# Optimization experiments

Measured on AMD Instinct MI355X. Metric: run time of the kernel, lower is better.

Reference implementation:

```python
import jax, jax.numpy as jnp
import numpy as np

BS, SEQ, VOCAB, EMS, NHID, ML = 32, 512, 5000, 256, 512, 16
TEMP = 0.9
GAMMA = 0.0  # self.gamma is a fixed zero Variable in the original


def setup_inputs() -> dict:
    key = jax.random.key(0)
    ks = jax.random.split(key, 10)
    nm = SEQ // ML
    inputs = jax.random.randint(ks[0], (BS, SEQ), 0, VOCAB, dtype=jnp.int32)
    measure_steps = jax.random.randint(ks[1], (ML, BS, nm), 0, VOCAB, dtype=jnp.int32)
    measure_weights = jax.random.normal(ks[2], (BS, nm, nm), dtype=jnp.float32)
    h0 = jnp.zeros((BS, NHID), jnp.float32)
    c0 = jnp.zeros((BS, NHID), jnp.float32)
    initrange = 0.1
    emb = jax.random.uniform(ks[3], (VOCAB, EMS), minval=-initrange, maxval=initrange)
    k = 1.0 / np.sqrt(NHID).astype(np.float32)
    W_ih = jax.random.uniform(ks[4], (4 * NHID, EMS), minval=-k, maxval=k)
    W_hh = jax.random.uniform(ks[5], (4 * NHID, NHID), minval=-k, maxval=k)
    b_ih = jax.random.uniform(ks[6], (4 * NHID,), minval=-k, maxval=k)
    b_hh = jax.random.uniform(ks[7], (4 * NHID,), minval=-k, maxval=k)
    W_dec = jax.random.uniform(ks[8], (VOCAB, NHID), minval=-initrange, maxval=initrange)
    b_dec = jnp.zeros((VOCAB,), jnp.float32)
    return dict(inputs=inputs, h0=h0, c0=c0, measure_weights=measure_weights,
                measure_steps=measure_steps, emb=emb, W_ih=W_ih, W_hh=W_hh,
                b_ih=b_ih, b_hh=b_hh, W_dec=W_dec, b_dec=b_dec, measure_length=ML)


def _forward(h0, c0, mw, emb, W_ih, W_hh, b_ih, b_hh, W_dec, b_dec,
             inputs, msteps, measure_length):
    bs, seq = inputs.shape
    nm = seq // measure_length
    # attention over previous measures: softmax over j < m (causal-masked)
    mask = (jnp.arange(nm)[None, :] < jnp.arange(nm)[:, None]).astype(mw.dtype)  # [m, j]
    logits = jnp.where(mask[None] > 0, mw / TEMP, -1e9)
    sm = jax.nn.softmax(logits, axis=-1) * mask[None]  # [bs, m, j]
    prev_embs = emb[msteps]  # [ML, bs, nm, E]
    # lookback embedding for (measure m, step s): sum_j sm[b,m,j] * emb[steps[s,b,j]]
    lb = jnp.einsum('bmj,sbje->msbe', sm, prev_embs)  # [nm, ML, bs, E]
    lb_seq = lb.reshape(seq, bs, -1)  # time-major: t = m*ML + s
    # per-step bmm decode against embedding table: [bs, seq, V]
    lookback = jnp.einsum('tbe,ve->btv', lb_seq, emb)
    # original zeros lookback for timesteps with int(i/num_measures)==0, i.e. i < nm
    tmask = (jnp.arange(seq) >= nm)[None, :, None]
    lookback = jnp.where(tmask, lookback, jnp.zeros((), lookback.dtype))

    x = emb[inputs]  # [bs, seq, E] (single channel -> concat is identity)

    def cell(carry, xt):
        h, c = carry
        g = xt @ W_ih.T + b_ih + h @ W_hh.T + b_hh
        i, f, gg, o = jnp.split(g, 4, axis=-1)
        c2 = jax.nn.sigmoid(f) * c + jax.nn.sigmoid(i) * jnp.tanh(gg)
        h2 = jax.nn.sigmoid(o) * jnp.tanh(c2)
        return (h2, c2), h2

    (hT, cT), hs = jax.lax.scan(cell, (h0, c0), jnp.swapaxes(x, 0, 1))
    out = jnp.swapaxes(hs, 0, 1)  # [bs, seq, nhid]
    decoded = out @ W_dec.T + b_dec  # [bs, seq, V]
    dec = (1.0 - GAMMA) * decoded + GAMMA * lookback
    return dec, hT, cT


def reference(inputs, h0, c0, measure_weights, measure_steps, emb,
              W_ih, W_hh, b_ih, b_hh, W_dec, b_dec, measure_length):
    return _forward(h0, c0, measure_weights, emb, W_ih, W_hh, b_ih, b_hh,
                    W_dec, b_dec, inputs, measure_steps, measure_length)
```

## Files before the change

### kernel.cpp

```cpp
#include <hip/hip_runtime.h>
#include <cstdint>
#include <cstddef>

#define BS     32
#define SEQ    512
#define VOCAB  5000
#define EMS    256
#define NHID   512
#define GH     2048
#define NWG    32
#define SLICE  16
#define VPAD   5120
#define NBLK   256
#define NDEC   (NBLK - NWG)
#define NTILE  ((BS*SEQ/128) * (VPAD/128))

#define WS_FLAGS 0
#define WS_BIAS  2048
#define WS_WIH   (WS_BIAS + GH*4)
#define WS_WHH   (WS_WIH + GH*EMS*2)
#define WS_WDH   (WS_WHH + GH*NHID*2)
#define WS_WDL   (WS_WDH + VPAD*NHID*2)
#define WS_X     (WS_WDL + VPAD*NHID*2)
#define WS_HHI   (WS_X + SEQ*BS*EMS*2)
#define WS_HLO   (WS_HHI + BS*SEQ*NHID*2)
#define WS_HBUF  (WS_HLO + BS*SEQ*NHID*2)
#define WS_END   (WS_HBUF + 2*BS*NHID*2)

typedef float f32x4 __attribute__((ext_vector_type(4)));
typedef __bf16 bf16x8 __attribute__((ext_vector_type(8)));

static __device__ __forceinline__ uint16_t f2bf(float x) {
  uint32_t u = __builtin_bit_cast(uint32_t, x);
  u += 0x7FFFu + ((u >> 16) & 1u);
  return (uint16_t)(u >> 16);
}
static __device__ __forceinline__ float bf2f(uint16_t b) {
  return __builtin_bit_cast(float, (uint32_t)b << 16);
}
static __device__ __forceinline__ float sigf(float x) { return 1.0f / (1.0f + __expf(-x)); }
static __device__ __forceinline__ float tanhf_fast(float x) {
  return 1.0f - 2.0f / (__expf(2.0f * x) + 1.0f);
}
static __device__ __forceinline__ f32x4 mfma16(uint4 a, uint4 b, f32x4 c) {
  return __builtin_amdgcn_mfma_f32_16x16x32_bf16(
      __builtin_bit_cast(bf16x8, a), __builtin_bit_cast(bf16x8, b), c, 0, 0, 0);
}
static __device__ __forceinline__ void glds16(const void* g, void* l) {
  __builtin_amdgcn_global_load_lds((__attribute__((address_space(1))) void*)g,
                                   (__attribute__((address_space(3))) void*)l,
                                   16, 0, 0);
}
static __device__ __forceinline__ void coh_store_u32(uint32_t* p, uint32_t v) {
  __hip_atomic_store(p, v, __ATOMIC_RELAXED, __HIP_MEMORY_SCOPE_AGENT);
}

__global__ __launch_bounds__(256) void prep_kernel(
    const int* __restrict__ inputs, const float* __restrict__ h0,
    const float* __restrict__ emb, const float* __restrict__ Wih,
    const float* __restrict__ Whh, const float* __restrict__ bih,
    const float* __restrict__ bhh, const float* __restrict__ Wd,
    char* __restrict__ ws) {
  int gid = blockIdx.x * 256 + threadIdx.x;
  int gsz = gridDim.x * 256;
  uint16_t* wX  = (uint16_t*)(ws + WS_X);
  uint16_t* wIH = (uint16_t*)(ws + WS_WIH);
  uint16_t* wHH = (uint16_t*)(ws + WS_WHH);
  uint16_t* wDH = (uint16_t*)(ws + WS_WDH);
  uint16_t* wDL = (uint16_t*)(ws + WS_WDL);
  float*    bias = (float*)(ws + WS_BIAS);
  uint16_t* hb  = (uint16_t*)(ws + WS_HBUF);
  if (gid < 512) ((uint32_t*)(ws + WS_FLAGS))[gid] = 0u;
  for (int i = gid; i < SEQ*BS*EMS; i += gsz) {
    int e = i & (EMS-1), b = (i >> 8) & (BS-1), t = i >> 13;
    wX[i] = f2bf(emb[(size_t)inputs[b*SEQ + t] * EMS + e]);
  }
  for (int i = gid; i < GH*EMS; i += gsz)  wIH[i] = f2bf(Wih[i]);
  for (int i = gid; i < GH*NHID; i += gsz) wHH[i] = f2bf(Whh[i]);
  for (int i = gid; i < VPAD*NHID; i += gsz) {
    int row = i >> 9;
    uint16_t hi = 0, lo = 0;
    if (row < VOCAB) {
      float x = Wd[i];
      hi = f2bf(x);
      lo = f2bf(x - bf2f(hi));
    }
    wDH[i] = hi; wDL[i] = lo;
  }
  for (int i = gid; i < GH; i += gsz) bias[i] = bih[i] + bhh[i];
  for (int i = gid; i < BS*NHID; i += gsz) hb[i] = f2bf(h0[i]);
}

__global__ __launch_bounds__(256, 1) void fused_kernel(
    char* __restrict__ ws, const float* __restrict__ c0,
    const float* __restrict__ bdec, float* __restrict__ out,
    float* __restrict__ outT) {
  __shared__ __align__(16) char smem[104 * 1024];
  uint32_t* flags = (uint32_t*)(ws + WS_FLAGS);
  const int tid = threadIdx.x;
  const int lane = tid & 63, w = tid >> 6;

  if (blockIdx.x < NWG) {
    char* sW = smem;
    char* sH = smem + 64*1024;
    float* sG = (float*)(smem + 96*1024);
    const uint16_t* wHH = (const uint16_t*)(ws + WS_WHH);
    const uint16_t* wIH = (const uint16_t*)(ws + WS_WIH);
    const uint16_t* wX  = (const uint16_t*)(ws + WS_X);
    const float* bias = (const float*)(ws + WS_BIAS);
    uint16_t* hbuf = (uint16_t*)(ws + WS_HBUF);
    uint16_t* Hhi  = (uint16_t*)(ws + WS_HHI);
    uint16_t* Hlo  = (uint16_t*)(ws + WS_HLO);
    const int wg = blockIdx.x;
    const int mw = w >> 1, nw = w & 1;

    for (int c = tid; c < 4096; c += 256) {
      int row = c >> 6;
      int kb = (c & 63) * 16;
      int G = row >> 4, dl = row & 15;
      uint4 v = *(const uint4*)(wHH + (size_t)(G*NHID + wg*SLICE + dl) * NHID + kb/2);
      *(uint4*)(sW + row*1024 + (kb ^ ((row & 7) << 4))) = v;
    }
    const int bq = tid >> 3, dq = (tid & 7) * 2;
    float c_0 = c0[bq*NHID + wg*SLICE + dq];
    float c_1 = c0[bq*NHID + wg*SLICE + dq + 1];
    const int arow = mw*16 + (lane & 15);
    const int brow0 = (2*nw)*16 + (lane & 15);
    const int brow1 = brow0 + 16;
    const int kb0 = (lane >> 4) * 16;
    const int kfrag = (lane >> 4) * 8;
    const float bs0 = bias[(2*nw+0)*NHID + wg*SLICE + (lane & 15)];
    const float bs1 = bias[(2*nw+1)*NHID + wg*SLICE + (lane & 15)];
    uint4 wbf[2][8];
#pragma unroll
    for (int g = 0; g < 2; ++g)
#pragma unroll
      for (int k2 = 0; k2 < 8; ++k2)
        wbf[g][k2] = *(const uint4*)(wIH +
            (size_t)((2*nw+g)*NHID + wg*SLICE + (lane & 15)) * EMS + k2*32 + kfrag);
    uint4 xa[8], xb[8];
#pragma unroll
    for (int k2 = 0; k2 < 8; ++k2)
      xa[k2] = *(const uint4*)(wX + (size_t)arow * EMS + k2*32 + kfrag);
    __syncthreads();

    for (int t = 0; t < SEQ; ++t) {
      if (t > 0) {
        const uint32_t tgt = (uint32_t)t;
        const uint32_t* fp = flags + (lane & 31) * 16;
        uint32_t ptries = 0;
        for (;;) {
          uint32_t v = __hip_atomic_load(fp, __ATOMIC_RELAXED, __HIP_MEMORY_SCOPE_AGENT);
          if (__all((int)(v >= tgt))) break;
          if (++ptries > (1u << 20)) break;
        }
      }

      uint4 v0, v1, v2, v3, v4, v5, v6, v7;
      {
        const char* pb = (const char*)(hbuf + (t & 1) * (BS*NHID)) + tid * 16;
        asm volatile("global_load_dwordx4 %0, %1, off sc0 sc1" : "=v"(v0) : "v"(pb));
        asm volatile("global_load_dwordx4 %0, %1, off sc0 sc1" : "=v"(v1) : "v"(pb + 4096));
        asm volatile("global_load_dwordx4 %0, %1, off sc0 sc1" : "=v"(v2) : "v"(pb + 8192));
        asm volatile("global_load_dwordx4 %0, %1, off sc0 sc1" : "=v"(v3) : "v"(pb + 12288));
        asm volatile("global_load_dwordx4 %0, %1, off sc0 sc1" : "=v"(v4) : "v"(pb + 16384));
        asm volatile("global_load_dwordx4 %0, %1, off sc0 sc1" : "=v"(v5) : "v"(pb + 20480));
        asm volatile("global_load_dwordx4 %0, %1, off sc0 sc1" : "=v"(v6) : "v"(pb + 24576));
        asm volatile("global_load_dwordx4 %0, %1, off sc0 sc1" : "=v"(v7) : "v"(pb + 28672));
        const int tn = (t + 1 < SEQ) ? (t + 1) : 0;
        const uint16_t* xp = wX + (size_t)(tn*BS + arow) * EMS + kfrag;
        asm volatile("global_load_dwordx4 %0, %1, off"             : "=v"(xb[0]) : "v"(xp));
        asm volatile("global_load_dwordx4 %0, %1, off offset:64"   : "=v"(xb[1]) : "v"(xp));
        asm volatile("global_load_dwordx4 %0, %1, off offset:128"  : "=v"(xb[2]) : "v"(xp));
        asm volatile("global_load_dwordx4 %0, %1, off offset:192"  : "=v"(xb[3]) : "v"(xp));
        asm volatile("global_load_dwordx4 %0, %1, off offset:256"  : "=v"(xb[4]) : "v"(xp));
        asm volatile("global_load_dwordx4 %0, %1, off offset:320"  : "=v"(xb[5]) : "v"(xp));
        asm volatile("global_load_dwordx4 %0, %1, off offset:384"  : "=v"(xb[6]) : "v"(xp));
        asm volatile("global_load_dwordx4 %0, %1, off offset:448"  : "=v"(xb[7]) : "v"(xp));
      }
      f32x4 acc0, acc1;
#pragma unroll
      for (int r = 0; r < 4; ++r) { acc0[r] = bs0; acc1[r] = bs1; }
#pragma unroll
      for (int k2 = 0; k2 < 8; ++k2) {
        acc0 = mfma16(xa[k2], wbf[0][k2], acc0);
        acc1 = mfma16(xa[k2], wbf[1][k2], acc1);
      }
      asm volatile("s_waitcnt vmcnt(8)" ::: "memory");
      __builtin_amdgcn_sched_barrier(0);
      {
        const int kb = (tid & 63) * 16;
        const int ww = tid >> 6;
#define STW(J, VJ) *(uint4*)(sH + ((J)*4 + ww)*1024 + (kb ^ ((((J)&1)*4 + ww) << 4))) = VJ;
        STW(0, v0) STW(1, v1) STW(2, v2) STW(3, v3)
        STW(4, v4) STW(5, v5) STW(6, v6) STW(7, v7)
#undef STW
      }
      __syncthreads();

#pragma unroll
      for (int kt = 0; kt < 16; ++kt) {
        int kb = kt*64 + kb0;
        uint4 av = *(const uint4*)(sH + arow*1024 + (kb ^ ((arow & 7) << 4)));
        uint4 b0 = *(const uint4*)(sW + brow0*1024 + (kb ^ ((brow0 & 7) << 4)));
        uint4 b1 = *(const uint4*)(sW + brow1*1024 + (kb ^ ((brow1 & 7) << 4)));
        acc0 = mfma16(av, b0, acc0);
        acc1 = mfma16(av, b1, acc1);
      }
#pragma unroll
      for (int r = 0; r < 4; ++r) {
        int b = mw*16 + (lane >> 4)*4 + r;
        sG[((2*nw+0)*BS + b)*SLICE + (lane & 15)] = acc0[r];
        sG[((2*nw+1)*BS + b)*SLICE + (lane & 15)] = acc1[r];
      }
#pragma unroll
      for (int k2 = 0; k2 < 8; ++k2) xa[k2] = xb[k2];
      __syncthreads();

      float gi0 = sG[(0*BS + bq)*SLICE + dq], gi1 = sG[(0*BS + bq)*SLICE + dq + 1];
      float gf0 = sG[(1*BS + bq)*SLICE + dq], gf1 = sG[(1*BS + bq)*SLICE + dq + 1];
      float gg0 = sG[(2*BS + bq)*SLICE + dq], gg1 = sG[(2*BS + bq)*SLICE + dq + 1];
      float go0 = sG[(3*BS + bq)*SLICE + dq], go1 = sG[(3*BS + bq)*SLICE + dq + 1];
      c_0 = sigf(gf0)*c_0 + sigf(gi0)*tanhf_fast(gg0);
      c_1 = sigf(gf1)*c_1 + sigf(gi1)*tanhf_fast(gg1);
      float h_0 = sigf(go0)*tanhf_fast(c_0);
      float h_1 = sigf(go1)*tanhf_fast(c_1);

      uint16_t hh0 = f2bf(h_0), hh1 = f2bf(h_1);
      uint32_t hp = (uint32_t)hh0 | ((uint32_t)hh1 << 16);
      coh_store_u32((uint32_t*)(hbuf + ((t+1) & 1)*(BS*NHID)) +
                        ((bq*NHID + wg*SLICE + dq) >> 1), hp);
      size_t hoff = ((size_t)t*BS + bq)*NHID + wg*SLICE + dq;
      coh_store_u32((uint32_t*)(Hhi + hoff), hp);
      uint32_t lp = (uint32_t)f2bf(h_0 - bf2f(hh0)) | ((uint32_t)f2bf(h_1 - bf2f(hh1)) << 16);
      coh_store_u32((uint32_t*)(Hlo + hoff), lp);
      if (t == SEQ-1) {
        outT[bq*NHID + wg*SLICE + dq]     = h_0;
        outT[bq*NHID + wg*SLICE + dq + 1] = h_1;
        outT[BS*NHID + bq*NHID + wg*SLICE + dq]     = c_0;
        outT[BS*NHID + bq*NHID + wg*SLICE + dq + 1] = c_1;
      }

      __syncthreads();
      if (tid == 0)
        __hip_atomic_store(flags + wg * 16, (uint32_t)(t + 1),
                           __ATOMIC_RELAXED, __HIP_MEMORY_SCOPE_AGENT);
    }
  } else {
    char* lds = smem;
    const uint16_t* Hhi = (const uint16_t*)(ws + WS_HHI);
    const uint16_t* Hlo = (const uint16_t*)(ws + WS_HLO);
    const uint16_t* WDH = (const uint16_t*)(ws + WS_WDH);
    const uint16_t* WDL = (const uint16_t*)(ws + WS_WDL);
    const uint16_t* As[3] = {Hhi, Hhi, Hlo};
    const uint16_t* Bs[3] = {WDH, WDL, WDH};
    const int widx = (int)blockIdx.x - NWG;
    const int wbase = (tid & ~63);
    const int mq = (w >> 1) * 64, nq = (w & 1) * 64;

    for (int q = widx; q < NTILE; q += NDEC) {
      const int mt = q / 40, nt = q % 40;
      const int m0 = mt * 128, n0 = nt * 128;
      if (w == 0) {
        const uint32_t tgt = (uint32_t)(mt*4 + 4);
        const uint32_t* fp = flags + (lane & 31) * 16;
        uint32_t tries = 0;
        for (;;) {
          uint32_t v = __hip_atomic_load(fp, __ATOMIC_RELAXED, __HIP_MEMORY_SCOPE_AGENT);
          if (__all((int)(v >= tgt))) break;
          __builtin_amdgcn_s_sleep(16);
          if (++tries > (1u << 15)) break;
        }
      }
      __syncthreads();

      auto stage = [&](int buf, int s) {
        const int p = s >> 4, kk = s & 15;
        const uint16_t* A = As[p];
        const uint16_t* B = Bs[p];
        char* dA = lds + buf*16384;
        char* dB = lds + buf*16384 + 8192;
#pragma unroll
        for (int c2 = 0; c2 < 2; ++c2) {
          int idx = c2*256 + tid;
          int row = idx >> 2, col = (idx & 3) * 8;
          glds16(A + (size_t)(m0 + row) * NHID + kk*32 + col, dA + (c2*256 + wbase)*16);
          glds16(B + (size_t)(n0 + row) * NHID + kk*32 + col, dB + (c2*256 + wbase)*16);
        }
      };

      const f32x4 zero = {0.f, 0.f, 0.f, 0.f};
      f32x4 acc[4][4];
#pragma unroll
      for (int i = 0; i < 4; ++i)
#pragma unroll
        for (int j = 0; j < 4; ++j) acc[i][j] = zero;

      stage(0, 0);
      for (int s = 0; s < 48; ++s) {
        __syncthreads();
        if (s + 1 < 48) stage((s + 1) & 1, s + 1);
        const char* cA = lds + (s & 1)*16384;
        const char* cB = lds + (s & 1)*16384 + 8192;
        uint4 a[4], b[4];
#pragma unroll
        for (int i = 0; i < 4; ++i) {
          a[i] = *(const uint4*)(cA + (mq + i*16 + (lane & 15))*64 + (lane >> 4)*16);
          b[i] = *(const uint4*)(cB + (nq + i*16 + (lane & 15))*64 + (lane >> 4)*16);
        }
#pragma unroll
        for (int i = 0; i < 4; ++i)
#pragma unroll
          for (int j = 0; j < 4; ++j) acc[i][j] = mfma16(a[i], b[j], acc[i][j]);
      }
#pragma unroll
      for (int j = 0; j < 4; ++j) {
        int V = n0 + nq + j*16 + (lane & 15);
        if (V >= VOCAB) continue;
        float bv = bdec[V];
#pragma unroll
        for (int i = 0; i < 4; ++i) {
          int Rb = m0 + mq + i*16 + (lane >> 4)*4;
#pragma unroll
          for (int r = 0; r < 4; ++r) {
            int rr = Rb + r;
            int orow = (rr & 31) * SEQ + (rr >> 5);
            out[(size_t)orow * VOCAB + V] = acc[i][j][r] + bv;
          }
        }
      }
      __syncthreads();
    }
  }
}

extern "C" void kernel_launch(void* const* d_in, const int* in_sizes, int n_in,
                              void* d_out, int out_size, void* d_ws, size_t ws_size,
                              hipStream_t stream) {
  (void)in_sizes; (void)n_in; (void)out_size; (void)ws_size;
  const int*   inputs = (const int*)  d_in[0];
  const float* h0     = (const float*)d_in[1];
  const float* c0     = (const float*)d_in[2];
  const float* emb    = (const float*)d_in[5];
  const float* Wih    = (const float*)d_in[6];
  const float* Whh    = (const float*)d_in[7];
  const float* bih    = (const float*)d_in[8];
  const float* bhh    = (const float*)d_in[9];
  const float* Wdec   = (const float*)d_in[10];
  const float* bdec   = (const float*)d_in[11];
  char* ws   = (char*)d_ws;
  float* out = (float*)d_out;
  float* outT = out + (size_t)BS*SEQ*VOCAB;

  prep_kernel<<<512, 256, 0, stream>>>(inputs, h0, emb, Wih, Whh, bih, bhh, Wdec, ws);
  fused_kernel<<<NBLK, 256, 0, stream>>>(ws, c0, bdec, out, outT);
}
```

Before: 2.102 ms.

## Stage hi and lo split operands together per K-step in decoder GEMM

The decoder GEMM used to make three separate passes over K, one for each bf16 split product (hi*hi, hi*lo, lo*hi), and each pass reloaded its A and B tiles. Now each K-step stages all four tiles (Hhi, Hlo, WDH, WDL) at once into a 32KB double buffer and issues the three MFMAs back to back. This cuts loop iterations and barriers by a factor of three and reuses Hhi and WDH across products. In exchange it doubles LDS per block and raises register pressure, which could lower occupancy. The spin-wait sleep interval and retry limit also change.

```diff
diff --git a/kernel.cpp b/kernel.cpp
--- a/kernel.cpp
+++ b/kernel.cpp
@@ -252,8 +252,6 @@
     const uint16_t* Hlo = (const uint16_t*)(ws + WS_HLO);
     const uint16_t* WDH = (const uint16_t*)(ws + WS_WDH);
     const uint16_t* WDL = (const uint16_t*)(ws + WS_WDL);
-    const uint16_t* As[3] = {Hhi, Hhi, Hlo};
-    const uint16_t* Bs[3] = {WDH, WDL, WDH};
     const int widx = (int)blockIdx.x - NWG;
     const int wbase = (tid & ~63);
     const int mq = (w >> 1) * 64, nq = (w & 1) * 64;
@@ -268,24 +266,23 @@
         for (;;) {
           uint32_t v = __hip_atomic_load(fp, __ATOMIC_RELAXED, __HIP_MEMORY_SCOPE_AGENT);
           if (__all((int)(v >= tgt))) break;
-          __builtin_amdgcn_s_sleep(16);
-          if (++tries > (1u << 15)) break;
-        }
-      }
-      __syncthreads();
-
-      auto stage = [&](int buf, int s) {
-        const int p = s >> 4, kk = s & 15;
-        const uint16_t* A = As[p];
-        const uint16_t* B = Bs[p];
-        char* dA = lds + buf*16384;
-        char* dB = lds + buf*16384 + 8192;
+          __builtin_amdgcn_s_sleep(64);
+          if (++tries > (1u << 14)) break;
+        }
+      }
+      __syncthreads();
+
+      auto stage = [&](int buf, int kk) {
+        char* base = lds + buf * 32768;
 #pragma unroll
         for (int c2 = 0; c2 < 2; ++c2) {
           int idx = c2*256 + tid;
           int row = idx >> 2, col = (idx & 3) * 8;
-          glds16(A + (size_t)(m0 + row) * NHID + kk*32 + col, dA + (c2*256 + wbase)*16);
-          glds16(B + (size_t)(n0 + row) * NHID + kk*32 + col, dB + (c2*256 + wbase)*16);
+          int ldst = (c2*256 + wbase) * 16;
+          glds16(Hhi + (size_t)(m0 + row) * NHID + kk*32 + col, base + ldst);
+          glds16(Hlo + (size_t)(m0 + row) * NHID + kk*32 + col, base + 8192 + ldst);
+          glds16(WDH + (size_t)(n0 + row) * NHID + kk*32 + col, base + 16384 + ldst);
+          glds16(WDL + (size_t)(n0 + row) * NHID + kk*32 + col, base + 24576 + ldst);
         }
       };
 
@@ -297,21 +294,28 @@
         for (int j = 0; j < 4; ++j) acc[i][j] = zero;
 
       stage(0, 0);
-      for (int s = 0; s < 48; ++s) {
+      for (int s = 0; s < 16; ++s) {
         __syncthreads();
-        if (s + 1 < 48) stage((s + 1) & 1, s + 1);
-        const char* cA = lds + (s & 1)*16384;
-        const char* cB = lds + (s & 1)*16384 + 8192;
-        uint4 a[4], b[4];
+        if (s + 1 < 16) stage((s + 1) & 1, s + 1);
+        const char* cb = lds + (s & 1) * 32768;
+        uint4 ahi[4], alo[4], bhi[4], blo[4];
 #pragma unroll
         for (int i = 0; i < 4; ++i) {
-          a[i] = *(const uint4*)(cA + (mq + i*16 + (lane & 15))*64 + (lane >> 4)*16);
-          b[i] = *(const uint4*)(cB + (nq + i*16 + (lane & 15))*64 + (lane >> 4)*16);
+          int aoff = (mq + i*16 + (lane & 15))*64 + (lane >> 4)*16;
+          int boff = (nq + i*16 + (lane & 15))*64 + (lane >> 4)*16;
+          ahi[i] = *(const uint4*)(cb + aoff);
+          alo[i] = *(const uint4*)(cb + 8192 + aoff);
+          bhi[i] = *(const uint4*)(cb + 16384 + boff);
+          blo[i] = *(const uint4*)(cb + 24576 + boff);
         }
 #pragma unroll
         for (int i = 0; i < 4; ++i)
 #pragma unroll
-          for (int j = 0; j < 4; ++j) acc[i][j] = mfma16(a[i], b[j], acc[i][j]);
+          for (int j = 0; j < 4; ++j) {
+            acc[i][j] = mfma16(ahi[i], bhi[j], acc[i][j]);
+            acc[i][j] = mfma16(ahi[i], blo[j], acc[i][j]);
+            acc[i][j] = mfma16(alo[i], bhi[j], acc[i][j]);
+          }
       }
 #pragma unroll
       for (int j = 0; j < 4; ++j) {
```

Result: no change. 2.085 ms (-0.8%).
